# Optimization experiments

Hardware: AMD Instinct MI355X
Metric: run time of the kernel (lower is better)

The kernel has to match this reference:

```python
import jax, jax.numpy as jnp
import numpy as np

N = 100000   # num nodes
E = 1200000  # num edges
D = 64       # embedding dim
K = 3        # propagation hops (alpha has K+1 entries)


def setup_inputs() -> dict:
    key = jax.random.key(0)
    k1, k2, k3 = jax.random.split(key, 3)
    edge_index = jax.random.randint(k1, (2, E), 0, N, dtype=jnp.int64)
    weight = jax.random.normal(k2, (N, D), dtype=jnp.float32)
    alpha = jax.random.uniform(k3, (K + 1,), dtype=jnp.float32)
    return {"edge_index": edge_index, "weight": weight, "alpha": alpha}


def reference(edge_index, weight, alpha):
    row = edge_index[0]  # source j
    col = edge_index[1]  # target i
    # symmetric normalization: in-degree over col, deg^-1/2 with inf -> 0
    deg = jax.ops.segment_sum(jnp.ones((E,), dtype=weight.dtype), col, num_segments=N)
    dinv = jnp.where(deg == 0, 0.0, deg ** -0.5)
    edge_w = dinv[row] * dinv[col]  # [E]

    out = weight * alpha[0]
    x = weight
    for k in range(1, K + 1):
        # gather-scale-scatter propagation hop
        msg = edge_w[:, None] * x[row]                      # [E, D]
        x = jax.ops.segment_sum(msg, col, num_segments=N)   # [N, D]
        out = out + x * alpha[k]

    # per-edge link scores: dot(out[src], out[dst])
    return jnp.sum(out[row] * out[col], axis=-1)  # [E]
```

## Files before the change

kernel.cpp:

```cpp
#include <hip/hip_runtime.h>
#include <hip/hip_bf16.h>

#define GN 100000
#define GE 1200000
#define GD 64
#define NG 256
#define CPG 391
#define CAP 6144


__global__ void detect_kernel(const void* __restrict__ w,
                              const void* __restrict__ edge,
                              int* __restrict__ flags, int* __restrict__ gcount) {
    __shared__ int s_badw, s_edgenz;
    if (threadIdx.x == 0) { s_badw = 0; s_edgenz = 0; }
    gcount[threadIdx.x] = 0;
    __syncthreads();
    const unsigned short* wh = (const unsigned short*)w;
    const unsigned int*   ei = (const unsigned int*)edge;
    int badw = 0, edgenz = 0;
    for (int i = threadIdx.x; i < 4096; i += 256) {
        unsigned int bits = ((unsigned int)wh[i]) << 16;
        float v = __uint_as_float(bits);
        if (!(fabsf(v) <= 100.0f)) badw = 1;
        if ((i & 1) == 1 && ei[i] != 0u) edgenz = 1;
    }
    if (badw)   atomicOr(&s_badw, 1);
    if (edgenz) atomicOr(&s_edgenz, 1);
    __syncthreads();
    if (threadIdx.x == 0) {
        flags[0] = s_badw ? 0 : 1;
        flags[1] = s_edgenz ? 0 : 1;
    }
}

__device__ __forceinline__ int ld_row(const int* __restrict__ edge, int e, int e64) {
    return e64 ? edge[2 * (size_t)e] : edge[e];
}
__device__ __forceinline__ int ld_col(const int* __restrict__ edge, int e, int e64) {
    return e64 ? edge[2 * ((size_t)GE + (size_t)e)] : edge[(size_t)GE + (size_t)e];
}
__device__ __forceinline__ float ld_f(const void* __restrict__ p, size_t i, int bf16f) {
    if (bf16f) return __bfloat162float(((const __hip_bfloat16*)p)[i]);
    return ((const float*)p)[i];
}

__device__ __forceinline__ float bf_lo(unsigned u) { return __uint_as_float(u << 16); }
__device__ __forceinline__ float bf_hi(unsigned u) { return __uint_as_float(u & 0xFFFF0000u); }
__device__ __forceinline__ unsigned bf16bits(float f) {
    __hip_bfloat16 h = __float2bfloat16(f);
    unsigned short s;
    __builtin_memcpy(&s, &h, 2);
    return (unsigned)s;
}

__global__ void p1init_kernel(const int* __restrict__ edge, const int* __restrict__ flags,
                              int* __restrict__ gcount, unsigned* __restrict__ bucket,
                              int E, int chunk,
                              const void* __restrict__ w, const void* __restrict__ alpha,
                              __hip_bfloat16* __restrict__ OUT, int nd) {
    if (blockIdx.x < NG) {
        __shared__ int cnt[NG];
        __shared__ int base[NG];
        int t = threadIdx.x;
        int e64 = flags[1];
        cnt[t] = 0;
        __syncthreads();
        int lo = blockIdx.x * chunk;
        int hiE = min(lo + chunk, E);
        for (int e = lo + t; e < hiE; e += 256) {
            int c = ld_col(edge, e, e64);
            int r = ld_row(edge, e, e64);
            if ((unsigned)c < (unsigned)GN && (unsigned)r < (unsigned)GN)
                atomicAdd(&cnt[c / CPG], 1);
        }
        __syncthreads();
        int cv = cnt[t];
        base[t] = (cv > 0) ? atomicAdd(&gcount[t], cv) : 0;
        __syncthreads();
        cnt[t] = 0;
        __syncthreads();
        for (int e = lo + t; e < hiE; e += 256) {
            int c = ld_col(edge, e, e64);
            int r = ld_row(edge, e, e64);
            if ((unsigned)c < (unsigned)GN && (unsigned)r < (unsigned)GN) {
                int g = c / CPG;
                int idx = base[g] + atomicAdd(&cnt[g], 1);
                if (idx < CAP)
                    bucket[(size_t)g * CAP + idx] = ((unsigned)(c - g * CPG) << 17) | (unsigned)r;
            }
        }
    } else {
        int bid = blockIdx.x - NG;
        int i = 4 * (bid * 256 + (int)threadIdx.x);
        int wbf = flags[0];
        if (i < nd) {
            float a0 = ld_f(alpha, 0, wbf);
            float v0 = ld_f(w, i + 0, wbf);
            float v1 = ld_f(w, i + 1, wbf);
            float v2 = ld_f(w, i + 2, wbf);
            float v3 = ld_f(w, i + 3, wbf);
            uint2 oq;
            oq.x = (bf16bits(a0 * v1) << 16) | bf16bits(a0 * v0);
            oq.y = (bf16bits(a0 * v3) << 16) | bf16bits(a0 * v2);
            *(uint2*)(OUT + i) = oq;
        }
    }
}

__global__ void p2_kernel(const unsigned* __restrict__ bucket, const int* __restrict__ gcount,
                          int* __restrict__ rowptr, float* __restrict__ dinv,
                          int* __restrict__ csr,
                          const void* __restrict__ w, const int* __restrict__ flags,
                          __hip_bfloat16* __restrict__ XS) {
    int g = blockIdx.x;
    int t = threadIdx.x;
    __shared__ int gs[NG];
    __shared__ int hist[512];
    __shared__ int s[512];
    __shared__ float sdv[512];
    int gv = gcount[t]; if (gv > CAP) gv = CAP;
    gs[t] = gv;
    hist[t] = 0; hist[t + 256] = 0;
    __syncthreads();
    for (int off = 1; off < NG; off <<= 1) {
        int u = (t >= off) ? gs[t - off] : 0;
        __syncthreads();
        gs[t] += u;
        __syncthreads();
    }
    int mg = gcount[g]; if (mg > CAP) mg = CAP;
    int gb = gs[g] - mg;
    int m = mg;
    const unsigned* bk = bucket + (size_t)g * CAP;
    for (int idx = t; idx < m; idx += 256)
        atomicAdd(&hist[bk[idx] >> 17], 1);
    __syncthreads();
    int h0 = hist[t], h1 = hist[t + 256];
    s[t] = h0; s[t + 256] = h1;
    __syncthreads();
    for (int off = 1; off < 512; off <<= 1) {
        int v0 = (t >= off) ? s[t - off] : 0;
        int v1 = (t + 256 >= off) ? s[t + 256 - off] : 0;
        __syncthreads();
        s[t] += v0; s[t + 256] += v1;
        __syncthreads();
    }
    float dv0 = (h0 > 0) ? rsqrtf((float)h0) : 0.0f;
    float dv1 = (h1 > 0) ? rsqrtf((float)h1) : 0.0f;
    sdv[t] = dv0; sdv[t + 256] = dv1;
    int col0 = g * CPG + t;
    int col1 = col0 + 256;
    if (col0 < GN) {
        rowptr[col0] = gb + s[t];
        dinv[col0] = dv0;
    }
    if (t + 256 < CPG && col1 < GN) {
        rowptr[col1] = gb + s[t + 256];
        dinv[col1] = dv1;
    }
    __syncthreads();
    hist[t] = s[t] - h0;
    hist[t + 256] = s[t + 256] - h1;
    __syncthreads();
    for (int idx = t; idx < m; idx += 256) {
        unsigned u = bk[idx];
        int cl = u >> 17;
        int r  = (int)(u & 0x1FFFFu);
        int pos = gb + atomicAdd(&hist[cl], 1);
        csr[pos] = r << 7;
    }
    int lo = g * CPG;
    int ncols = min(CPG, GN - lo);
    int tot = ncols << 6;
    int wbf = flags[0];
    size_t gbase = (size_t)lo << 6;
    if (wbf) {
        const unsigned short* wp = (const unsigned short*)w;
        for (int idx = 4 * t; idx < tot; idx += 1024) {
            float dv = sdv[idx >> 6];
            size_t base = gbase + (size_t)idx;
            uint2 wv = *(const uint2*)(wp + base);
            uint2 o;
            o.x = (bf16bits(dv * bf_hi(wv.x)) << 16) | bf16bits(dv * bf_lo(wv.x));
            o.y = (bf16bits(dv * bf_hi(wv.y)) << 16) | bf16bits(dv * bf_lo(wv.y));
            *(uint2*)(XS + base) = o;
        }
    } else {
        const float* wp = (const float*)w;
        for (int idx = 4 * t; idx < tot; idx += 1024) {
            float dv = sdv[idx >> 6];
            size_t base = gbase + (size_t)idx;
            float4 wv = *(const float4*)(wp + base);
            uint2 o;
            o.x = (bf16bits(dv * wv.y) << 16) | bf16bits(dv * wv.x);
            o.y = (bf16bits(dv * wv.w) << 16) | bf16bits(dv * wv.z);
            *(uint2*)(XS + base) = o;
        }
    }
}

__global__ void gather_kernel(const __hip_bfloat16* __restrict__ XS,
                              __hip_bfloat16* __restrict__ Y,
                              __hip_bfloat16* __restrict__ OUT,
                              const int* __restrict__ rowptr, const int* __restrict__ csr,
                              const float* __restrict__ dinv,
                              const void* __restrict__ alpha, const int* __restrict__ flags,
                              int k, int store_y, int N) {
    int t = blockIdx.x * blockDim.x + threadIdx.x;
    int node = __builtin_amdgcn_readfirstlane(t >> 6);
    if (node >= N) return;
    int lane = t & 63;
    int h = lane >> 4;
    int i = lane & 15;
    int beg = node ? rowptr[node - 1] : 0;
    int end = rowptr[node];
    float dc = dinv[node];
    float a = ld_f(alpha, k, flags[0]);
    size_t obase = (size_t)node * GD + 4 * i;
    uint2 uo = *(const uint2*)(OUT + obase);
    const char* xb = (const char*)XS;
    unsigned ioff = 8u * (unsigned)i;
    int last = end - 1;
    float f0 = 0.0f, f1 = 0.0f, f2 = 0.0f, f3 = 0.0f;
    for (int j = beg; j < end; j += 16) {
        int i0 = j + 0 + h;  int i1 = j + 4 + h;
        int i2 = j + 8 + h;  int i3 = j + 12 + h;
        unsigned r0 = (unsigned)csr[min(i0, last)];
        unsigned r1 = (unsigned)csr[min(i1, last)];
        unsigned r2 = (unsigned)csr[min(i2, last)];
        unsigned r3 = (unsigned)csr[min(i3, last)];
        float w0 = (i0 < end) ? 1.0f : 0.0f;
        float w1 = (i1 < end) ? 1.0f : 0.0f;
        float w2 = (i2 < end) ? 1.0f : 0.0f;
        float w3 = (i3 < end) ? 1.0f : 0.0f;
        uint2 u0 = *(const uint2*)(xb + (r0 + ioff));
        uint2 u1 = *(const uint2*)(xb + (r1 + ioff));
        uint2 u2 = *(const uint2*)(xb + (r2 + ioff));
        uint2 u3 = *(const uint2*)(xb + (r3 + ioff));
        f0 = fmaf(w0, bf_lo(u0.x), f0); f1 = fmaf(w0, bf_hi(u0.x), f1);
        f2 = fmaf(w0, bf_lo(u0.y), f2); f3 = fmaf(w0, bf_hi(u0.y), f3);
        f0 = fmaf(w1, bf_lo(u1.x), f0); f1 = fmaf(w1, bf_hi(u1.x), f1);
        f2 = fmaf(w1, bf_lo(u1.y), f2); f3 = fmaf(w1, bf_hi(u1.y), f3);
        f0 = fmaf(w2, bf_lo(u2.x), f0); f1 = fmaf(w2, bf_hi(u2.x), f1);
        f2 = fmaf(w2, bf_lo(u2.y), f2); f3 = fmaf(w2, bf_hi(u2.y), f3);
        f0 = fmaf(w3, bf_lo(u3.x), f0); f1 = fmaf(w3, bf_hi(u3.x), f1);
        f2 = fmaf(w3, bf_lo(u3.y), f2); f3 = fmaf(w3, bf_hi(u3.y), f3);
    }
    f0 += __shfl_xor(f0, 16, 64); f0 += __shfl_xor(f0, 32, 64);
    f1 += __shfl_xor(f1, 16, 64); f1 += __shfl_xor(f1, 32, 64);
    f2 += __shfl_xor(f2, 16, 64); f2 += __shfl_xor(f2, 32, 64);
    f3 += __shfl_xor(f3, 16, 64); f3 += __shfl_xor(f3, 32, 64);
    f0 *= dc; f1 *= dc; f2 *= dc; f3 *= dc;
    if (h == 0) {
        if (store_y) {
            uint2 p;
            p.x = (bf16bits(dc * f1) << 16) | bf16bits(dc * f0);
            p.y = (bf16bits(dc * f3) << 16) | bf16bits(dc * f2);
            *(uint2*)(Y + obase) = p;
        }
        float o0 = fmaf(a, f0, bf_lo(uo.x));
        float o1 = fmaf(a, f1, bf_hi(uo.x));
        float o2 = fmaf(a, f2, bf_lo(uo.y));
        float o3 = fmaf(a, f3, bf_hi(uo.y));
        uint2 q;
        q.x = (bf16bits(o1) << 16) | bf16bits(o0);
        q.y = (bf16bits(o3) << 16) | bf16bits(o2);
        *(uint2*)(OUT + obase) = q;
    }
}

__device__ __forceinline__ float dot2_bf16(unsigned ua, unsigned ub) {
    return fmaf(bf_lo(ua), bf_lo(ub), bf_hi(ua) * bf_hi(ub));
}

__global__ void dot_kernel(const __hip_bfloat16* __restrict__ OUT,
                           const int* __restrict__ edge, const int* __restrict__ flags,
                           void* __restrict__ res, int E) {
    int t = blockIdx.x * blockDim.x + threadIdx.x;
    int e = t >> 2;
    int sub = t & 3;
    if (e >= E) return;
    int e64 = flags[1];
    int wbf = flags[0];
    int r = ld_row(edge, e, e64);
    int c = ld_col(edge, e, e64);
    float p = 0.0f;
    if ((unsigned)r < (unsigned)GN && (unsigned)c < (unsigned)GN) {
        const uint4* pa = (const uint4*)(OUT + (size_t)r * GD + sub * 16);
        const uint4* pb = (const uint4*)(OUT + (size_t)c * GD + sub * 16);
        uint4 a0 = pa[0], a1 = pa[1];
        uint4 b0 = pb[0], b1 = pb[1];
        p = ((dot2_bf16(a0.x, b0.x) + dot2_bf16(a0.y, b0.y)) +
             (dot2_bf16(a0.z, b0.z) + dot2_bf16(a0.w, b0.w))) +
            ((dot2_bf16(a1.x, b1.x) + dot2_bf16(a1.y, b1.y)) +
             (dot2_bf16(a1.z, b1.z) + dot2_bf16(a1.w, b1.w)));
    }
    p += __shfl_down(p, 2, 4);
    p += __shfl_down(p, 1, 4);
    if (sub == 0) {
        if (wbf) ((__hip_bfloat16*)res)[e] = __float2bfloat16(p);
        else     ((float*)res)[e] = p;
    }
}

extern "C" void kernel_launch(void* const* d_in, const int* in_sizes, int n_in,
                              void* d_out, int out_size, void* d_ws, size_t ws_size,
                              hipStream_t stream) {
    const int E = GE, N = GN, ND = GN * GD;

    const void* edge   = d_in[0];
    const void* weight = d_in[1];
    const void* alpha  = d_in[2];

    char* ws = (char*)d_ws;
    int*      flags     = (int*)ws;      ws += 256;
    int*      gcount    = (int*)ws;      ws += 1024;
    float*    dinv      = (float*)ws;    ws += (((size_t)N * 4 + 255) / 256) * 256;
    int*      rowptr    = (int*)ws;      ws += (((size_t)N * 4 + 255) / 256) * 256;
    unsigned* bucket    = (unsigned*)ws; ws += (size_t)NG * CAP * 4;
    int*      csr       = (int*)ws;      ws += (size_t)E * 4;
    __hip_bfloat16* X   = (__hip_bfloat16*)ws; ws += (size_t)ND * 2;
    __hip_bfloat16* Y   = (__hip_bfloat16*)ws; ws += (size_t)ND * 2;
    __hip_bfloat16* OUT = (__hip_bfloat16*)ws; ws += (size_t)ND * 2;

    const int B = 256;

    detect_kernel<<<1, 256, 0, stream>>>(weight, edge, flags, gcount);

    {
        const int chunk = (E + NG - 1) / NG;
        const int initBlocks = (ND / 4 + B - 1) / B;
        p1init_kernel<<<NG + initBlocks, B, 0, stream>>>(
            (const int*)edge, flags, gcount, bucket, E, chunk,
            weight, alpha, OUT, ND);
    }
    p2_kernel<<<NG, 256, 0, stream>>>(bucket, gcount, rowptr, dinv, csr,
                                      weight, flags, X);

    const int ggrid = (int)(((size_t)N * 64 + B - 1) / B);
    gather_kernel<<<ggrid, B, 0, stream>>>(X, Y, OUT, rowptr, csr, dinv, alpha, flags, 1, 1, N);
    gather_kernel<<<ggrid, B, 0, stream>>>(Y, X, OUT, rowptr, csr, dinv, alpha, flags, 2, 1, N);
    gather_kernel<<<ggrid, B, 0, stream>>>(X, Y, OUT, rowptr, csr, dinv, alpha, flags, 3, 0, N);

    dot_kernel<<<(int)(((size_t)E * 4 + B - 1) / B), B, 0, stream>>>(OUT, (const int*)edge, flags, d_out, E);
}
```

Before: 259.3 us.

## Pad CSR segments to 16 with zero-row sentinel and coalesce index loads via shuffles

```diff
diff --git a/kernel.cpp b/kernel.cpp
--- a/kernel.cpp
+++ b/kernel.cpp
@@ -7,14 +7,23 @@
 #define NG 256
 #define CPG 391
 #define CAP 6144
+#define PADCAP 12032
+#define ZROFF (GN << 7)
 
 
 __global__ void detect_kernel(const void* __restrict__ w,
                               const void* __restrict__ edge,
-                              int* __restrict__ flags, int* __restrict__ gcount) {
+                              int* __restrict__ flags, int* __restrict__ gcount,
+                              __hip_bfloat16* __restrict__ X,
+                              __hip_bfloat16* __restrict__ Y) {
     __shared__ int s_badw, s_edgenz;
     if (threadIdx.x == 0) { s_badw = 0; s_edgenz = 0; }
     gcount[threadIdx.x] = 0;
+    if (threadIdx.x < 16) {
+        uint2 z; z.x = 0u; z.y = 0u;
+        *(uint2*)(X + (size_t)GN * GD + 4 * threadIdx.x) = z;
+        *(uint2*)(Y + (size_t)GN * GD + 4 * threadIdx.x) = z;
+    }
     __syncthreads();
     const unsigned short* wh = (const unsigned short*)w;
     const unsigned int*   ei = (const unsigned int*)edge;
@@ -109,35 +118,26 @@
 }
 
 __global__ void p2_kernel(const unsigned* __restrict__ bucket, const int* __restrict__ gcount,
-                          int* __restrict__ rowptr, float* __restrict__ dinv,
+                          int2* __restrict__ begend, float* __restrict__ dinv,
                           int* __restrict__ csr,
                           const void* __restrict__ w, const int* __restrict__ flags,
                           __hip_bfloat16* __restrict__ XS) {
     int g = blockIdx.x;
     int t = threadIdx.x;
-    __shared__ int gs[NG];
     __shared__ int hist[512];
     __shared__ int s[512];
     __shared__ float sdv[512];
-    int gv = gcount[t]; if (gv > CAP) gv = CAP;
-    gs[t] = gv;
     hist[t] = 0; hist[t + 256] = 0;
     __syncthreads();
-    for (int off = 1; off < NG; off <<= 1) {
-        int u = (t >= off) ? gs[t - off] : 0;
-        __syncthreads();
-        gs[t] += u;
-        __syncthreads();
-    }
     int mg = gcount[g]; if (mg > CAP) mg = CAP;
-    int gb = gs[g] - mg;
-    int m = mg;
     const unsigned* bk = bucket + (size_t)g * CAP;
-    for (int idx = t; idx < m; idx += 256)
+    for (int idx = t; idx < mg; idx += 256)
         atomicAdd(&hist[bk[idx] >> 17], 1);
     __syncthreads();
     int h0 = hist[t], h1 = hist[t + 256];
-    s[t] = h0; s[t + 256] = h1;
+    int p0 = (h0 + 15) & ~15;
+    int p1 = (h1 + 15) & ~15;
+    s[t] = p0; s[t + 256] = p1;
     __syncthreads();
     for (int off = 1; off < 512; off <<= 1) {
         int v0 = (t >= off) ? s[t - off] : 0;
@@ -146,30 +146,37 @@
         s[t] += v0; s[t + 256] += v1;
         __syncthreads();
     }
+    int gb = g * PADCAP;
+    int beg0 = gb + s[t] - p0;
+    int beg1 = gb + s[t + 256] - p1;
     float dv0 = (h0 > 0) ? rsqrtf((float)h0) : 0.0f;
     float dv1 = (h1 > 0) ? rsqrtf((float)h1) : 0.0f;
     sdv[t] = dv0; sdv[t + 256] = dv1;
     int col0 = g * CPG + t;
     int col1 = col0 + 256;
     if (col0 < GN) {
-        rowptr[col0] = gb + s[t];
+        begend[col0] = make_int2(beg0, beg0 + p0);
         dinv[col0] = dv0;
     }
     if (t + 256 < CPG && col1 < GN) {
-        rowptr[col1] = gb + s[t + 256];
+        begend[col1] = make_int2(beg1, beg1 + p1);
         dinv[col1] = dv1;
     }
     __syncthreads();
-    hist[t] = s[t] - h0;
-    hist[t + 256] = s[t + 256] - h1;
-    __syncthreads();
-    for (int idx = t; idx < m; idx += 256) {
+    hist[t] = s[t] - p0;
+    hist[t + 256] = s[t + 256] - p1;
+    __syncthreads();
+    for (int idx = t; idx < mg; idx += 256) {
         unsigned u = bk[idx];
         int cl = u >> 17;
         int r  = (int)(u & 0x1FFFFu);
         int pos = gb + atomicAdd(&hist[cl], 1);
         csr[pos] = r << 7;
     }
+    if (col0 < GN)
+        for (int q = h0; q < p0; ++q) csr[beg0 + q] = ZROFF;
+    if (t + 256 < CPG && col1 < GN)
+        for (int q = h1; q < p1; ++q) csr[beg1 + q] = ZROFF;
     int lo = g * CPG;
     int ncols = min(CPG, GN - lo);
     int tot = ncols << 6;
@@ -203,7 +210,7 @@
 __global__ void gather_kernel(const __hip_bfloat16* __restrict__ XS,
                               __hip_bfloat16* __restrict__ Y,
                               __hip_bfloat16* __restrict__ OUT,
-                              const int* __restrict__ rowptr, const int* __restrict__ csr,
+                              const int2* __restrict__ begend, const int* __restrict__ csr,
                               const float* __restrict__ dinv,
                               const void* __restrict__ alpha, const int* __restrict__ flags,
                               int k, int store_y, int N) {
@@ -213,39 +220,29 @@
     int lane = t & 63;
     int h = lane >> 4;
     int i = lane & 15;
-    int beg = node ? rowptr[node - 1] : 0;
-    int end = rowptr[node];
+    int2 be = begend[node];
+    int beg = be.x, end = be.y;
     float dc = dinv[node];
     float a = ld_f(alpha, k, flags[0]);
     size_t obase = (size_t)node * GD + 4 * i;
     uint2 uo = *(const uint2*)(OUT + obase);
     const char* xb = (const char*)XS;
     unsigned ioff = 8u * (unsigned)i;
-    int last = end - 1;
     float f0 = 0.0f, f1 = 0.0f, f2 = 0.0f, f3 = 0.0f;
     for (int j = beg; j < end; j += 16) {
-        int i0 = j + 0 + h;  int i1 = j + 4 + h;
-        int i2 = j + 8 + h;  int i3 = j + 12 + h;
-        unsigned r0 = (unsigned)csr[min(i0, last)];
-        unsigned r1 = (unsigned)csr[min(i1, last)];
-        unsigned r2 = (unsigned)csr[min(i2, last)];
-        unsigned r3 = (unsigned)csr[min(i3, last)];
-        float w0 = (i0 < end) ? 1.0f : 0.0f;
-        float w1 = (i1 < end) ? 1.0f : 0.0f;
-        float w2 = (i2 < end) ? 1.0f : 0.0f;
-        float w3 = (i3 < end) ? 1.0f : 0.0f;
+        int rv = csr[j + i];
+        unsigned r0 = (unsigned)__shfl(rv, h,      16);
+        unsigned r1 = (unsigned)__shfl(rv, 4 + h,  16);
+        unsigned r2 = (unsigned)__shfl(rv, 8 + h,  16);
+        unsigned r3 = (unsigned)__shfl(rv, 12 + h, 16);
         uint2 u0 = *(const uint2*)(xb + (r0 + ioff));
         uint2 u1 = *(const uint2*)(xb + (r1 + ioff));
         uint2 u2 = *(const uint2*)(xb + (r2 + ioff));
         uint2 u3 = *(const uint2*)(xb + (r3 + ioff));
-        f0 = fmaf(w0, bf_lo(u0.x), f0); f1 = fmaf(w0, bf_hi(u0.x), f1);
-        f2 = fmaf(w0, bf_lo(u0.y), f2); f3 = fmaf(w0, bf_hi(u0.y), f3);
-        f0 = fmaf(w1, bf_lo(u1.x), f0); f1 = fmaf(w1, bf_hi(u1.x), f1);
-        f2 = fmaf(w1, bf_lo(u1.y), f2); f3 = fmaf(w1, bf_hi(u1.y), f3);
-        f0 = fmaf(w2, bf_lo(u2.x), f0); f1 = fmaf(w2, bf_hi(u2.x), f1);
-        f2 = fmaf(w2, bf_lo(u2.y), f2); f3 = fmaf(w2, bf_hi(u2.y), f3);
-        f0 = fmaf(w3, bf_lo(u3.x), f0); f1 = fmaf(w3, bf_hi(u3.x), f1);
-        f2 = fmaf(w3, bf_lo(u3.y), f2); f3 = fmaf(w3, bf_hi(u3.y), f3);
+        f0 += bf_lo(u0.x); f1 += bf_hi(u0.x); f2 += bf_lo(u0.y); f3 += bf_hi(u0.y);
+        f0 += bf_lo(u1.x); f1 += bf_hi(u1.x); f2 += bf_lo(u1.y); f3 += bf_hi(u1.y);
+        f0 += bf_lo(u2.x); f1 += bf_hi(u2.x); f2 += bf_lo(u2.y); f3 += bf_hi(u2.y);
+        f0 += bf_lo(u3.x); f1 += bf_hi(u3.x); f2 += bf_lo(u3.y); f3 += bf_hi(u3.y);
     }
     f0 += __shfl_xor(f0, 16, 64); f0 += __shfl_xor(f0, 32, 64);
     f1 += __shfl_xor(f1, 16, 64); f1 += __shfl_xor(f1, 32, 64);
@@ -308,6 +305,7 @@
                               void* d_out, int out_size, void* d_ws, size_t ws_size,
                               hipStream_t stream) {
     const int E = GE, N = GN, ND = GN * GD;
+    const int NDP = (GN + 1) * GD;
 
     const void* edge   = d_in[0];
     const void* weight = d_in[1];
@@ -317,16 +315,16 @@
     int*      flags     = (int*)ws;      ws += 256;
     int*      gcount    = (int*)ws;      ws += 1024;
     float*    dinv      = (float*)ws;    ws += (((size_t)N * 4 + 255) / 256) * 256;
-    int*      rowptr    = (int*)ws;      ws += (((size_t)N * 4 + 255) / 256) * 256;
+    int2*     begend    = (int2*)ws;     ws += (((size_t)N * 8 + 255) / 256) * 256;
     unsigned* bucket    = (unsigned*)ws; ws += (size_t)NG * CAP * 4;
-    int*      csr       = (int*)ws;      ws += (size_t)E * 4;
-    __hip_bfloat16* X   = (__hip_bfloat16*)ws; ws += (size_t)ND * 2;
-    __hip_bfloat16* Y   = (__hip_bfloat16*)ws; ws += (size_t)ND * 2;
+    int*      csr       = (int*)ws;      ws += (size_t)NG * PADCAP * 4;
+    __hip_bfloat16* X   = (__hip_bfloat16*)ws; ws += (size_t)NDP * 2;
+    __hip_bfloat16* Y   = (__hip_bfloat16*)ws; ws += (size_t)NDP * 2;
     __hip_bfloat16* OUT = (__hip_bfloat16*)ws; ws += (size_t)ND * 2;
 
     const int B = 256;
 
-    detect_kernel<<<1, 256, 0, stream>>>(weight, edge, flags, gcount);
+    detect_kernel<<<1, 256, 0, stream>>>(weight, edge, flags, gcount, X, Y);
 
     {
         const int chunk = (E + NG - 1) / NG;
@@ -335,13 +333,13 @@
             (const int*)edge, flags, gcount, bucket, E, chunk,
             weight, alpha, OUT, ND);
     }
-    p2_kernel<<<NG, 256, 0, stream>>>(bucket, gcount, rowptr, dinv, csr,
+    p2_kernel<<<NG, 256, 0, stream>>>(bucket, gcount, begend, dinv, csr,
                                       weight, flags, X);
 
     const int ggrid = (int)(((size_t)N * 64 + B - 1) / B);
-    gather_kernel<<<ggrid, B, 0, stream>>>(X, Y, OUT, rowptr, csr, dinv, alpha, flags, 1, 1, N);
-    gather_kernel<<<ggrid, B, 0, stream>>>(Y, X, OUT, rowptr, csr, dinv, alpha, flags, 2, 1, N);
-    gather_kernel<<<ggrid, B, 0, stream>>>(X, Y, OUT, rowptr, csr, dinv, alpha, flags, 3, 0, N);
+    gather_kernel<<<ggrid, B, 0, stream>>>(X, Y, OUT, begend, csr, dinv, alpha, flags, 1, 1, N);
+    gather_kernel<<<ggrid, B, 0, stream>>>(Y, X, OUT, begend, csr, dinv, alpha, flags, 2, 1, N);
+    gather_kernel<<<ggrid, B, 0, stream>>>(X, Y, OUT, begend, csr, dinv, alpha, flags, 3, 0, N);
 
     dot_kernel<<<(int)(((size_t)E * 4 + B - 1) / B), B, 0, stream>>>(OUT, (const int*)edge, flags, d_out, E);
 }
```

Result: no change. 259.0 us (-0.1%).
